# Optimization experiments

Hardware: AMD Instinct MI355X
Metric: run time of the kernel (lower is better)

Reference implementation:

```python
import jax, jax.numpy as jnp
import numpy as np

DIM = 1024
HEADS = 16
HEAD_DIM = DIM // HEADS
HIDDEN = 4 * DIM
EPS = 1e-5


def _layernorm(x, g, b):
    m = jnp.mean(x, axis=-1, keepdims=True)
    v = jnp.mean((x - m) ** 2, axis=-1, keepdims=True)
    return (x - m) * jax.lax.rsqrt(v + EPS) * g + b


def setup_inputs() -> dict:
    key = jax.random.key(0)
    ks = jax.random.split(key, 8)
    s = 0.02
    return {
        "x": jax.random.normal(ks[0], (16, 577, DIM), dtype=jnp.float32),
        "w_qkv": jax.random.normal(ks[1], (3 * DIM, DIM), dtype=jnp.float32) * s,
        "b_qkv": jnp.zeros((3 * DIM,), dtype=jnp.float32),
        "w_proj": jax.random.normal(ks[2], (DIM, DIM), dtype=jnp.float32) * s,
        "b_proj": jnp.zeros((DIM,), dtype=jnp.float32),
        "ln1_g": jnp.ones((DIM,), dtype=jnp.float32),
        "ln1_b": jnp.zeros((DIM,), dtype=jnp.float32),
        "ln2_g": jnp.ones((DIM,), dtype=jnp.float32),
        "ln2_b": jnp.zeros((DIM,), dtype=jnp.float32),
        "w_fc1": jax.random.normal(ks[3], (HIDDEN, DIM), dtype=jnp.float32) * s,
        "b_fc1": jnp.zeros((HIDDEN,), dtype=jnp.float32),
        "w_fc2": jax.random.normal(ks[4], (DIM, HIDDEN), dtype=jnp.float32) * s,
        "b_fc2": jnp.zeros((DIM,), dtype=jnp.float32),
    }


def reference(x, w_qkv, b_qkv, w_proj, b_proj, ln1_g, ln1_b, ln2_g, ln2_b,
              w_fc1, b_fc1, w_fc2, b_fc2):
    B, N, C = x.shape
    scale = HEAD_DIM ** -0.5
    # --- attention sub-block ---
    xn = _layernorm(x, ln1_g, ln1_b)
    qkv = xn @ w_qkv.T + b_qkv  # [B, N, 3C]
    qkv = qkv.reshape(B, N, 3, HEADS, HEAD_DIM)
    q = qkv[:, :, 0].transpose(0, 2, 1, 3)  # [B, H, N, D]
    k = qkv[:, :, 1].transpose(0, 2, 1, 3)
    v = qkv[:, :, 2].transpose(0, 2, 1, 3)
    attn = jnp.einsum('bhnd,bhmd->bhnm', q, k) * scale
    attn = jax.nn.softmax(attn, axis=-1)
    y = jnp.einsum('bhnm,bhmd->bhnd', attn, v)  # [B, H, N, D]
    y = y.transpose(0, 2, 1, 3).reshape(B, N, C)
    y = y @ w_proj.T + b_proj
    x = x + y
    # --- MLP sub-block ---
    xn2 = _layernorm(x, ln2_g, ln2_b)
    h = jax.nn.gelu(xn2 @ w_fc1.T + b_fc1, approximate=False)
    x = x + (h @ w_fc2.T + b_fc2)
    return x
```

## Files before the change

kernel.cpp:

```cpp
#include <hip/hip_runtime.h>
#include <cmath>


#define MTOK 9232
#define MPAD 9344
#define MT_TILES 73
#define SEQ  577
#define SEQP 640
#define NKT  10

typedef _Float16 half8  __attribute__((ext_vector_type(8)));
typedef _Float16 half4  __attribute__((ext_vector_type(4)));
typedef _Float16 half2v __attribute__((ext_vector_type(2)));
typedef __fp16   fp16x2 __attribute__((ext_vector_type(2)));
typedef float    float4v __attribute__((ext_vector_type(4)));

__device__ __forceinline__ void gl_lds16(const void* g, void* l) {
  __builtin_amdgcn_global_load_lds((const __attribute__((address_space(1))) void*)g,
                                   (__attribute__((address_space(3))) void*)l, 16, 0, 0);
}

__device__ __forceinline__ float fexp2(float x) { return __builtin_amdgcn_exp2f(x); }
__device__ __forceinline__ float frcp(float x)  { return __builtin_amdgcn_rcpf(x); }
__device__ __forceinline__ float bperm_f(int addr, float v) {
  return __int_as_float(__builtin_amdgcn_ds_bpermute(addr, __float_as_int(v)));
}
__device__ __forceinline__ half2v pack2(float a, float b) {
  fp16x2 p = __builtin_amdgcn_cvt_pkrtz(a, b);
  return __builtin_bit_cast(half2v, p);
}

__global__ __launch_bounds__(256) void cvt_all_kernel(const float* __restrict__ s0, _Float16* __restrict__ d0,
                                                      const float* __restrict__ s1, _Float16* __restrict__ d1,
                                                      const float* __restrict__ s2, _Float16* __restrict__ d2,
                                                      const float* __restrict__ s3, _Float16* __restrict__ d3) {
  int blk = blockIdx.x;
  const float* in; _Float16* out; int base;
  if (blk < 1536)      { in = s0; out = d0; base = blk; }
  else if (blk < 2048) { in = s1; out = d1; base = blk - 1536; }
  else if (blk < 4096) { in = s2; out = d2; base = blk - 2048; }
  else                 { in = s3; out = d3; base = blk - 4096; }
  int i = (base * 256 + threadIdx.x) * 8;
  float4v a = *(const float4v*)(in + i);
  float4v b = *(const float4v*)(in + i + 4);
  half8 o = { (_Float16)a[0], (_Float16)a[1], (_Float16)a[2], (_Float16)a[3],
              (_Float16)b[0], (_Float16)b[1], (_Float16)b[2], (_Float16)b[3] };
  *(half8*)(out + i) = o;
}

__global__ __launch_bounds__(256) void ln_kernel(const float* __restrict__ x,
                                                 const float* __restrict__ gam,
                                                 const float* __restrict__ bet,
                                                 _Float16* __restrict__ out, int mrows) {
  int row = blockIdx.x, t = threadIdx.x;
  _Float16* orow = out + (long)row * 1024 + t * 4;
  if (row >= mrows) { half4 z = {}; *(half4*)orow = z; return; }
  float4v xv = *(const float4v*)(x + (long)row * 1024 + t * 4);
  float s  = xv[0] + xv[1] + xv[2] + xv[3];
  float ss = xv[0]*xv[0] + xv[1]*xv[1] + xv[2]*xv[2] + xv[3]*xv[3];
  #pragma unroll
  for (int o = 32; o > 0; o >>= 1) { s += __shfl_down(s, o); ss += __shfl_down(ss, o); }
  __shared__ float red[8];
  int w = t >> 6;
  if ((t & 63) == 0) { red[w] = s; red[4 + w] = ss; }
  __syncthreads();
  s  = red[0] + red[1] + red[2] + red[3];
  ss = red[4] + red[5] + red[6] + red[7];
  float mean = s * (1.0f / 1024.0f);
  float var  = ss * (1.0f / 1024.0f) - mean * mean;
  float rstd = rsqrtf(var + 1e-5f);
  float4v gv = *(const float4v*)(gam + t * 4);
  float4v bv = *(const float4v*)(bet + t * 4);
  half4 o;
  #pragma unroll
  for (int i = 0; i < 4; i++) o[i] = (_Float16)((xv[i] - mean) * rstd * gv[i] + bv[i]);
  *(half4*)orow = o;
}

template <int EPI, int DBUF>
__global__ __launch_bounds__(256, DBUF ? 2 : 3)
void gemm_bt(const _Float16* __restrict__ A,
             const _Float16* __restrict__ Bw,
             const float* __restrict__ bias,
             const float* __restrict__ res,
             void* __restrict__ outv, int Ndim, int K) {
  __shared__ __align__(16) _Float16 SH[DBUF ? 32768 : 16384];
  const int GM = 16;
  int nTiles = Ndim >> 7;
  int per = GM * nTiles;
  int lin = blockIdx.x;
  int panel = lin / per;
  int rem = lin - panel * per;
  int gm = MT_TILES - panel * GM; if (gm > GM) gm = GM;
  int mt = panel * GM + rem % gm;
  int nt = rem / gm;
  int t = threadIdx.x, w = t >> 6, l = t & 63;
  int wm = (w >> 1) * 64, wn = (w & 1) * 64;
  int g = l >> 4, li = l & 15;
  float4v acc[4][4] = {};

  long soff[4];
  #pragma unroll
  for (int r = 0; r < 4; ++r) {
    int idx = (w * 4 + r) * 64 + l;
    int row = idx >> 3;
    int kc  = (idx & 7) ^ (row & 7);
    soff[r] = (long)row * K + kc * 8;
  }
  int aro[2][4], bro[2][4];
  #pragma unroll
  for (int ks = 0; ks < 2; ++ks) {
    #pragma unroll
    for (int i = 0; i < 4; ++i) {
      int ar = wm + i * 16 + li;
      aro[ks][i] = ar * 64 + (((ks * 4 + g) ^ (ar & 7)) * 8);
      int br = wn + i * 16 + li;
      bro[ks][i] = br * 64 + (((ks * 4 + g) ^ (br & 7)) * 8);
    }
  }

  const _Float16* ak = A  + (long)mt * 128 * K;
  const _Float16* bk = Bw + (long)nt * 128 * K;
  int nk = K >> 6;

  if (DBUF) {
    #pragma unroll
    for (int r = 0; r < 4; ++r) {
      gl_lds16(ak + soff[r], SH + (w * 4 + r) * 512);
      gl_lds16(bk + soff[r], SH + 8192 + (w * 4 + r) * 512);
    }
    ak += 64; bk += 64;
    for (int kt = 0; kt < nk; ++kt) {
      __syncthreads();
      int coff = (kt & 1) ? 16384 : 0;
      int noff = coff ^ 16384;
      if (kt + 1 < nk) {
        #pragma unroll
        for (int r = 0; r < 4; ++r) {
          gl_lds16(ak + soff[r], SH + noff + (w * 4 + r) * 512);
          gl_lds16(bk + soff[r], SH + noff + 8192 + (w * 4 + r) * 512);
        }
        ak += 64; bk += 64;
      }
      #pragma unroll
      for (int ks = 0; ks < 2; ++ks) {
        half8 af[4], bf[4];
        #pragma unroll
        for (int i = 0; i < 4; i++) af[i] = *(const half8*)(SH + coff + aro[ks][i]);
        #pragma unroll
        for (int j = 0; j < 4; j++) bf[j] = *(const half8*)(SH + coff + 8192 + bro[ks][j]);
        #pragma unroll
        for (int i = 0; i < 4; i++)
          #pragma unroll
          for (int j = 0; j < 4; j++)
            acc[i][j] = __builtin_amdgcn_mfma_f32_16x16x32_f16(af[i], bf[j], acc[i][j], 0, 0, 0);
      }
    }
    __syncthreads();
  } else {
    for (int kt = 0; kt < nk; ++kt) {
      #pragma unroll
      for (int r = 0; r < 4; ++r) {
        gl_lds16(ak + soff[r], SH + (w * 4 + r) * 512);
        gl_lds16(bk + soff[r], SH + 8192 + (w * 4 + r) * 512);
      }
      ak += 64; bk += 64;
      __syncthreads();
      #pragma unroll
      for (int ks = 0; ks < 2; ++ks) {
        half8 af[4], bf[4];
        #pragma unroll
        for (int i = 0; i < 4; i++) af[i] = *(const half8*)(SH + aro[ks][i]);
        #pragma unroll
        for (int j = 0; j < 4; j++) bf[j] = *(const half8*)(SH + 8192 + bro[ks][j]);
        #pragma unroll
        for (int i = 0; i < 4; i++)
          #pragma unroll
          for (int j = 0; j < 4; j++)
            acc[i][j] = __builtin_amdgcn_mfma_f32_16x16x32_f16(af[i], bf[j], acc[i][j], 0, 0, 0);
      }
      __syncthreads();
    }
  }

  if (EPI == 2) {
    float* Shf = (float*)SH;
    #pragma unroll
    for (int p = 0; p < 4; ++p) {
      if ((w & 1) == (p >> 1)) {
        int j0 = (p & 1) * 2;
        #pragma unroll
        for (int i = 0; i < 4; ++i) {
          #pragma unroll
          for (int jj = 0; jj < 2; ++jj) {
            #pragma unroll
            for (int r = 0; r < 4; ++r) {
              int row = wm + i * 16 + g * 4 + r;
              Shf[row * 36 + jj * 16 + li] = acc[i][j0 + jj][r];
            }
          }
        }
      }
      __syncthreads();
      #pragma unroll
      for (int it = 0; it < 4; ++it) {
        int chunk = it * 256 + t;
        int row = chunk >> 3, c4 = chunk & 7;
        int grow = mt * 128 + row;
        if (grow < MTOK) {
          float4v v = *(const float4v*)(Shf + row * 36 + c4 * 4);
          int gcol = nt * 128 + p * 32 + c4 * 4;
          float4v bv = *(const float4v*)(bias + gcol);
          float4v rv = *(const float4v*)(res + (long)grow * Ndim + gcol);
          v = v + bv + rv;
          *(float4v*)((float*)outv + (long)grow * Ndim + gcol) = v;
        }
      }
      __syncthreads();
    }
  } else {
    _Float16* Sh = SH;
    float bsv[4];
    #pragma unroll
    for (int j = 0; j < 4; ++j) bsv[j] = bias[nt * 128 + wn + j * 16 + li];
    #pragma unroll
    for (int p = 0; p < 2; ++p) {
      if ((w & 1) == p) {
        #pragma unroll
        for (int i = 0; i < 4; ++i) {
          int rl = (w >> 1) * 64 + i * 16 + g * 4;
          #pragma unroll
          for (int j = 0; j < 4; ++j) {
            #pragma unroll
            for (int r = 0; r < 4; ++r) {
              float v = acc[i][j][r] + bsv[j];
              if (EPI == 1) {
                float y = v * (0.79788456f + 0.035677408f * v * v);
                v = v * frcp(1.0f + fexp2(-2.88539008f * y));
              }
              Sh[(rl + r) * 68 + j * 16 + li] = (_Float16)v;
            }
          }
        }
      }
      __syncthreads();
      #pragma unroll
      for (int cc = 0; cc < 4; ++cc) {
        int chunk = cc * 256 + t;
        int row = chunk >> 3, kc8 = chunk & 7;
        half8 hv = *(const half8*)(Sh + row * 68 + kc8 * 8);
        *(half8*)((_Float16*)outv + (long)(mt * 128 + row) * Ndim + nt * 128 + p * 64 + kc8 * 8) = hv;
      }
      __syncthreads();
    }
  }
}

__global__ __launch_bounds__(256) void vt_kernel(const _Float16* __restrict__ qkv,
                                                 _Float16* __restrict__ Vt) {
  int kt = blockIdx.x, bh = blockIdx.y;
  int b = bh >> 4, h = bh & 15;
  long base = (long)b * SEQ;
  __shared__ _Float16 Lt[64][72];
  int t = threadIdx.x;
  #pragma unroll
  for (int c = t; c < 512; c += 256) {
    int key = c >> 3, dc = c & 7;
    int kglob = kt * 64 + key;
    half8 v = {};
    if (kglob < SEQ) v = *(const half8*)(qkv + (base + kglob) * 3072 + 2048 + h * 64 + dc * 8);
    *(half8*)(&Lt[key][dc * 8]) = v;
  }
  __syncthreads();
  #pragma unroll
  for (int c = t; c < 512; c += 256) {
    int d = c >> 3, kc = c & 7;
    half8 o;
    #pragma unroll
    for (int j = 0; j < 8; j++) o[j] = Lt[kc * 8 + j][d];
    *(half8*)(Vt + ((long)bh * 64 + d) * SEQP + kt * 64 + kc * 8) = o;
  }
}

__global__ __launch_bounds__(256, 4) void attn_kernel(const _Float16* __restrict__ qkv,
                                                      const _Float16* __restrict__ Vt,
                                                      _Float16* __restrict__ Y) {
  int bh = blockIdx.x, qt = blockIdx.y;
  int b = bh >> 4, h = bh & 15;
  long base = (long)b * SEQ;
  int t = threadIdx.x, w = t >> 6, l = t & 63;
  int g = l >> 4, li = l & 15;
  __shared__ __align__(16) _Float16 Ks[64 * 64];
  __shared__ __align__(16) _Float16 Vs[64 * 64];
  __shared__ __align__(16) _Float16 Pw[4][16 * 40];
  int q0 = qt * 64 + w * 16;
  half8 qf[2];
  #pragma unroll
  for (int ks = 0; ks < 2; ++ks)
    qf[ks] = *(const half8*)(qkv + (base + q0 + li) * 3072 + h * 64 + ks * 32 + g * 8);
  float4v o[4] = {};
  float mold = -1e30f, lsum = 0.f;
  int abase = (l & 48);
  const _Float16* vtb = Vt + (long)bh * 64 * SEQP;
  const float sc = 0.125f * 1.44269504f;
  for (int kt = 0; kt < NKT; ++kt) {
    #pragma unroll
    for (int rr = 0; rr < 2; ++rr) {
      int idx = rr * 256 + w * 64 + l;
      int row = idx >> 3;
      int kc  = (idx & 7) ^ (row & 7);
      gl_lds16(qkv + (base + kt * 64 + row) * 3072 + 1024 + h * 64 + kc * 8,
               Ks + (rr * 256 + w * 64) * 8);
      gl_lds16(vtb + (long)row * SEQP + kt * 64 + kc * 8,
               Vs + (rr * 256 + w * 64) * 8);
    }
    __syncthreads();
    float4v st[4] = {};
    #pragma unroll
    for (int ks = 0; ks < 2; ++ks) {
      #pragma unroll
      for (int mt = 0; mt < 4; ++mt) {
        int kr = mt * 16 + li;
        half8 kf = *(const half8*)(Ks + kr * 64 + (((ks * 4 + g) ^ (kr & 7)) * 8));
        st[mt] = __builtin_amdgcn_mfma_f32_16x16x32_f16(kf, qf[ks], st[mt], 0, 0, 0);
      }
    }
    bool last = (kt == NKT - 1);
    float mx = -1e30f;
    #pragma unroll
    for (int mt = 0; mt < 4; ++mt) {
      #pragma unroll
      for (int r = 0; r < 4; ++r) {
        float v = st[mt][r] * sc;
        if (last && (kt * 64 + mt * 16 + g * 4 + r) >= SEQ) v = -1e30f;
        st[mt][r] = v;
        mx = fmaxf(mx, v);
      }
    }
    mx = fmaxf(mx, __shfl_xor(mx, 16));
    mx = fmaxf(mx, __shfl_xor(mx, 32));
    float mnew = fmaxf(mold, mx);
    float alpha = fexp2(mold - mnew);
    mold = mnew;
    half2v pk[4][2];
    float psum = 0.f;
    #pragma unroll
    for (int mt = 0; mt < 4; ++mt) {
      float p0 = fexp2(st[mt][0] - mnew);
      float p1 = fexp2(st[mt][1] - mnew);
      float p2 = fexp2(st[mt][2] - mnew);
      float p3 = fexp2(st[mt][3] - mnew);
      psum += (p0 + p1) + (p2 + p3);
      pk[mt][0] = pack2(p0, p1);
      pk[mt][1] = pack2(p2, p3);
    }
    lsum = lsum * alpha + psum;
    float ab[4];
    #pragma unroll
    for (int r = 0; r < 4; ++r) ab[r] = bperm_f(abase + 4 * r, alpha);
    #pragma unroll
    for (int nd = 0; nd < 4; ++nd)
      #pragma unroll
      for (int r = 0; r < 4; ++r) o[nd][r] *= ab[r];
    #pragma unroll
    for (int ks = 0; ks < 2; ++ks) {
      #pragma unroll
      for (int mtl = 0; mtl < 2; ++mtl) {
        int mt = 2 * ks + mtl;
        *(half2v*)(&Pw[w][li * 40 + mtl * 16 + g * 4])     = pk[mt][0];
        *(half2v*)(&Pw[w][li * 40 + mtl * 16 + g * 4 + 2]) = pk[mt][1];
      }
      half8 pa = *(const half8*)(&Pw[w][li * 40 + g * 8]);
      #pragma unroll
      for (int nd = 0; nd < 4; ++nd) {
        int vr = nd * 16 + li;
        half8 vf = *(const half8*)(Vs + vr * 64 + (((ks * 4 + g) ^ (vr & 7)) * 8));
        o[nd] = __builtin_amdgcn_mfma_f32_16x16x32_f16(pa, vf, o[nd], 0, 0, 0);
      }
    }
    __syncthreads();
  }
  lsum += __shfl_xor(lsum, 16);
  lsum += __shfl_xor(lsum, 32);
  float linv = frcp(lsum);
  float lb[4];
  #pragma unroll
  for (int r = 0; r < 4; ++r) lb[r] = bperm_f(abase + 4 * r, linv);
  #pragma unroll
  for (int r = 0; r < 4; ++r) {
    int qr = qt * 64 + w * 16 + g * 4 + r;
    if (qr < SEQ) {
      _Float16* yp = Y + (base + qr) * 1024 + h * 64 + li;
      #pragma unroll
      for (int nd = 0; nd < 4; ++nd) yp[nd * 16] = (_Float16)(o[nd][r] * lb[r]);
    }
  }
}

extern "C" void kernel_launch(void* const* d_in, const int* in_sizes, int n_in,
                              void* d_out, int out_size, void* d_ws, size_t ws_size,
                              hipStream_t stream) {
  (void)in_sizes; (void)n_in; (void)out_size; (void)ws_size;
  const float* x      = (const float*)d_in[0];
  const float* w_qkv  = (const float*)d_in[1];
  const float* b_qkv  = (const float*)d_in[2];
  const float* w_proj = (const float*)d_in[3];
  const float* b_proj = (const float*)d_in[4];
  const float* ln1_g  = (const float*)d_in[5];
  const float* ln1_b  = (const float*)d_in[6];
  const float* ln2_g  = (const float*)d_in[7];
  const float* ln2_b  = (const float*)d_in[8];
  const float* w_fc1  = (const float*)d_in[9];
  const float* b_fc1  = (const float*)d_in[10];
  const float* w_fc2  = (const float*)d_in[11];
  const float* b_fc2  = (const float*)d_in[12];

  char* ws = (char*)d_ws;
  _Float16* Abuf = (_Float16*)ws;
  _Float16* Wq   = (_Float16*)(ws + 19136512);
  _Float16* Wp   = Wq + 3072 * 1024;
  _Float16* W1   = Wp + 1024 * 1024;
  _Float16* W2   = W1 + 4096 * 1024;
  _Float16* Qb   = (_Float16*)(ws + 44302336);
  _Float16* Yb   = Qb + (long)MPAD * 3072;
  _Float16* Hb   = Qb;
  float*    X1   = (float*)(ws + 120848384);
  _Float16* Vtb  = (_Float16*)(ws + 120848384);

  cvt_all_kernel<<<6144, 256, 0, stream>>>(w_qkv, Wq, w_proj, Wp, w_fc1, W1, w_fc2, W2);

  ln_kernel<<<MPAD, 256, 0, stream>>>(x, ln1_g, ln1_b, Abuf, MTOK);
  gemm_bt<0, 0><<<73 * 24, 256, 0, stream>>>(Abuf, Wq, b_qkv, nullptr, Qb, 3072, 1024);
  vt_kernel<<<dim3(NKT, 256), 256, 0, stream>>>(Qb, Vtb);
  attn_kernel<<<dim3(256, NKT), 256, 0, stream>>>(Qb, Vtb, Yb);
  gemm_bt<2, 1><<<73 * 8, 256, 0, stream>>>(Yb, Wp, b_proj, x, X1, 1024, 1024);
  ln_kernel<<<MPAD, 256, 0, stream>>>(X1, ln2_g, ln2_b, Abuf, MTOK);
  gemm_bt<1, 0><<<73 * 32, 256, 0, stream>>>(Abuf, W1, b_fc1, nullptr, Hb, 4096, 1024);
  gemm_bt<2, 1><<<73 * 8, 256, 0, stream>>>(Hb, W2, b_fc2, X1, d_out, 1024, 4096);
}
```

Measured before the change: 552.2 us.

## Use 128x64 single-buffered tiles for N=1024 residual GEMMs

Adds a new GEMM kernel with 128x64 output tiles, smaller LDS, and four blocks per CU for the proj and fc2 GEMMs. It replaces the double-buffered 128x128 variant and doubles the block count (73*16 instead of 73*8) so the 256 CUs are better filled. The aim is to fix low occupancy and wave quantization on the N=1024 GEMMs. The cost is losing the double-buffered prefetch and re-reading A tiles more often.

```diff
diff --git a/kernel.cpp b/kernel.cpp
--- a/kernel.cpp
+++ b/kernel.cpp
@@ -77,14 +77,12 @@
   *(half4*)orow = o;
 }
 
-template <int EPI, int DBUF>
-__global__ __launch_bounds__(256, DBUF ? 2 : 3)
-void gemm_bt(const _Float16* __restrict__ A,
-             const _Float16* __restrict__ Bw,
-             const float* __restrict__ bias,
-             const float* __restrict__ res,
-             void* __restrict__ outv, int Ndim, int K) {
-  __shared__ __align__(16) _Float16 SH[DBUF ? 32768 : 16384];
+template <int EPI>
+__global__ __launch_bounds__(256, 3) void gemm_bt(const _Float16* __restrict__ A,
+                                                  const _Float16* __restrict__ Bw,
+                                                  const float* __restrict__ bias,
+                                                  void* __restrict__ outv, int Ndim, int K) {
+  __shared__ __align__(16) _Float16 SH[16384];
   const int GM = 16;
   int nTiles = Ndim >> 7;
   int per = GM * nTiles;
@@ -122,137 +120,172 @@
   const _Float16* ak = A  + (long)mt * 128 * K;
   const _Float16* bk = Bw + (long)nt * 128 * K;
   int nk = K >> 6;
-
-  if (DBUF) {
+  for (int kt = 0; kt < nk; ++kt) {
     #pragma unroll
     for (int r = 0; r < 4; ++r) {
       gl_lds16(ak + soff[r], SH + (w * 4 + r) * 512);
       gl_lds16(bk + soff[r], SH + 8192 + (w * 4 + r) * 512);
     }
     ak += 64; bk += 64;
-    for (int kt = 0; kt < nk; ++kt) {
-      __syncthreads();
-      int coff = (kt & 1) ? 16384 : 0;
-      int noff = coff ^ 16384;
-      if (kt + 1 < nk) {
+    __syncthreads();
+    #pragma unroll
+    for (int ks = 0; ks < 2; ++ks) {
+      half8 af[4], bf[4];
+      #pragma unroll
+      for (int i = 0; i < 4; i++) af[i] = *(const half8*)(SH + aro[ks][i]);
+      #pragma unroll
+      for (int j = 0; j < 4; j++) bf[j] = *(const half8*)(SH + 8192 + bro[ks][j]);
+      #pragma unroll
+      for (int i = 0; i < 4; i++)
         #pragma unroll
-        for (int r = 0; r < 4; ++r) {
-          gl_lds16(ak + soff[r], SH + noff + (w * 4 + r) * 512);
-          gl_lds16(bk + soff[r], SH + noff + 8192 + (w * 4 + r) * 512);
-        }
-        ak += 64; bk += 64;
-      }
-      #pragma unroll
-      for (int ks = 0; ks < 2; ++ks) {
-        half8 af[4], bf[4];
+        for (int j = 0; j < 4; j++)
+          acc[i][j] = __builtin_amdgcn_mfma_f32_16x16x32_f16(af[i], bf[j], acc[i][j], 0, 0, 0);
+    }
+    __syncthreads();
+  }
+  _Float16* Sh = SH;
+  float bsv[4];
+  #pragma unroll
+  for (int j = 0; j < 4; ++j) bsv[j] = bias[nt * 128 + wn + j * 16 + li];
+  #pragma unroll
+  for (int p = 0; p < 2; ++p) {
+    if ((w & 1) == p) {
+      #pragma unroll
+      for (int i = 0; i < 4; ++i) {
+        int rl = (w >> 1) * 64 + i * 16 + g * 4;
         #pragma unroll
-        for (int i = 0; i < 4; i++) af[i] = *(const half8*)(SH + coff + aro[ks][i]);
-        #pragma unroll
-        for (int j = 0; j < 4; j++) bf[j] = *(const half8*)(SH + coff + 8192 + bro[ks][j]);
-        #pragma unroll
-        for (int i = 0; i < 4; i++)
+        for (int j = 0; j < 4; ++j) {
           #pragma unroll
-          for (int j = 0; j < 4; j++)
-            acc[i][j] = __builtin_amdgcn_mfma_f32_16x16x32_f16(af[i], bf[j], acc[i][j], 0, 0, 0);
-      }
-    }
-    __syncthreads();
-  } else {
-    for (int kt = 0; kt < nk; ++kt) {
-      #pragma unroll
-      for (int r = 0; r < 4; ++r) {
-        gl_lds16(ak + soff[r], SH + (w * 4 + r) * 512);
-        gl_lds16(bk + soff[r], SH + 8192 + (w * 4 + r) * 512);
-      }
-      ak += 64; bk += 64;
-      __syncthreads();
-      #pragma unroll
-      for (int ks = 0; ks < 2; ++ks) {
-        half8 af[4], bf[4];
-        #pragma unroll
-        for (int i = 0; i < 4; i++) af[i] = *(const half8*)(SH + aro[ks][i]);
-        #pragma unroll
-        for (int j = 0; j < 4; j++) bf[j] = *(const half8*)(SH + 8192 + bro[ks][j]);
-        #pragma unroll
-        for (int i = 0; i < 4; i++)
-          #pragma unroll
-          for (int j = 0; j < 4; j++)
-            acc[i][j] = __builtin_amdgcn_mfma_f32_16x16x32_f16(af[i], bf[j], acc[i][j], 0, 0, 0);
-      }
-      __syncthreads();
-    }
-  }
-
-  if (EPI == 2) {
-    float* Shf = (float*)SH;
-    #pragma unroll
-    for (int p = 0; p < 4; ++p) {
-      if ((w & 1) == (p >> 1)) {
-        int j0 = (p & 1) * 2;
-        #pragma unroll
-        for (int i = 0; i < 4; ++i) {
-          #pragma unroll
-          for (int jj = 0; jj < 2; ++jj) {
-            #pragma unroll
-            for (int r = 0; r < 4; ++r) {
-              int row = wm + i * 16 + g * 4 + r;
-              Shf[row * 36 + jj * 16 + li] = acc[i][j0 + jj][r];
+          for (int r = 0; r < 4; ++r) {
+            float v = acc[i][j][r] + bsv[j];
+            if (EPI == 1) {
+              float y = v * (0.79788456f + 0.035677408f * v * v);
+              v = v * frcp(1.0f + fexp2(-2.88539008f * y));
             }
+            Sh[(rl + r) * 68 + j * 16 + li] = (_Float16)v;
           }
         }
       }
-      __syncthreads();
-      #pragma unroll
-      for (int it = 0; it < 4; ++it) {
-        int chunk = it * 256 + t;
-        int row = chunk >> 3, c4 = chunk & 7;
-        int grow = mt * 128 + row;
-        if (grow < MTOK) {
-          float4v v = *(const float4v*)(Shf + row * 36 + c4 * 4);
-          int gcol = nt * 128 + p * 32 + c4 * 4;
-          float4v bv = *(const float4v*)(bias + gcol);
-          float4v rv = *(const float4v*)(res + (long)grow * Ndim + gcol);
-          v = v + bv + rv;
-          *(float4v*)((float*)outv + (long)grow * Ndim + gcol) = v;
-        }
-      }
-      __syncthreads();
-    }
-  } else {
-    _Float16* Sh = SH;
-    float bsv[4];
-    #pragma unroll
-    for (int j = 0; j < 4; ++j) bsv[j] = bias[nt * 128 + wn + j * 16 + li];
-    #pragma unroll
-    for (int p = 0; p < 2; ++p) {
-      if ((w & 1) == p) {
+    }
+    __syncthreads();
+    #pragma unroll
+    for (int cc = 0; cc < 4; ++cc) {
+      int chunk = cc * 256 + t;
+      int row = chunk >> 3, kc8 = chunk & 7;
+      half8 hv = *(const half8*)(Sh + row * 68 + kc8 * 8);
+      *(half8*)((_Float16*)outv + (long)(mt * 128 + row) * Ndim + nt * 128 + p * 64 + kc8 * 8) = hv;
+    }
+    __syncthreads();
+  }
+}
+
+__global__ __launch_bounds__(256, 4) void gemm_bt64(const _Float16* __restrict__ A,
+                                                    const _Float16* __restrict__ Bw,
+                                                    const float* __restrict__ bias,
+                                                    const float* __restrict__ res,
+                                                    float* __restrict__ outv, int Ndim, int K) {
+  __shared__ __align__(16) _Float16 SH[12288];
+  const int GM = 16;
+  int nTiles = Ndim >> 6;
+  int per = GM * nTiles;
+  int lin = blockIdx.x;
+  int panel = lin / per;
+  int rem = lin - panel * per;
+  int gm = MT_TILES - panel * GM; if (gm > GM) gm = GM;
+  int mt = panel * GM + rem % gm;
+  int nt = rem / gm;
+  int t = threadIdx.x, w = t >> 6, l = t & 63;
+  int wm = (w >> 1) * 64, wn = (w & 1) * 32;
+  int g = l >> 4, li = l & 15;
+  float4v acc[4][2] = {};
+
+  long soffA[4], soffB[2];
+  #pragma unroll
+  for (int r = 0; r < 4; ++r) {
+    int idx = (w * 4 + r) * 64 + l;
+    int row = idx >> 3;
+    int kc  = (idx & 7) ^ (row & 7);
+    soffA[r] = (long)row * K + kc * 8;
+  }
+  #pragma unroll
+  for (int r = 0; r < 2; ++r) {
+    int idx = (w * 2 + r) * 64 + l;
+    int row = idx >> 3;
+    int kc  = (idx & 7) ^ (row & 7);
+    soffB[r] = (long)row * K + kc * 8;
+  }
+  int aro[2][4], bro[2][2];
+  #pragma unroll
+  for (int ks = 0; ks < 2; ++ks) {
+    #pragma unroll
+    for (int i = 0; i < 4; ++i) {
+      int ar = wm + i * 16 + li;
+      aro[ks][i] = ar * 64 + (((ks * 4 + g) ^ (ar & 7)) * 8);
+    }
+    #pragma unroll
+    for (int j = 0; j < 2; ++j) {
+      int br = wn + j * 16 + li;
+      bro[ks][j] = br * 64 + (((ks * 4 + g) ^ (br & 7)) * 8);
+    }
+  }
+
+  const _Float16* ak = A  + (long)mt * 128 * K;
+  const _Float16* bk = Bw + (long)nt * 64 * K;
+  int nk = K >> 6;
+  for (int kt = 0; kt < nk; ++kt) {
+    #pragma unroll
+    for (int r = 0; r < 4; ++r) gl_lds16(ak + soffA[r], SH + (w * 4 + r) * 512);
+    #pragma unroll
+    for (int r = 0; r < 2; ++r) gl_lds16(bk + soffB[r], SH + 8192 + (w * 2 + r) * 512);
+    ak += 64; bk += 64;
+    __syncthreads();
+    #pragma unroll
+    for (int ks = 0; ks < 2; ++ks) {
+      half8 af[4], bf[2];
+      #pragma unroll
+      for (int i = 0; i < 4; i++) af[i] = *(const half8*)(SH + aro[ks][i]);
+      #pragma unroll
+      for (int j = 0; j < 2; j++) bf[j] = *(const half8*)(SH + 8192 + bro[ks][j]);
+      #pragma unroll
+      for (int i = 0; i < 4; i++)
         #pragma unroll
-        for (int i = 0; i < 4; ++i) {
-          int rl = (w >> 1) * 64 + i * 16 + g * 4;
+        for (int j = 0; j < 2; j++)
+          acc[i][j] = __builtin_amdgcn_mfma_f32_16x16x32_f16(af[i], bf[j], acc[i][j], 0, 0, 0);
+    }
+    __syncthreads();
+  }
+  float* Shf = (float*)SH;
+  #pragma unroll
+  for (int p = 0; p < 2; ++p) {
+    if ((w & 1) == p) {
+      #pragma unroll
+      for (int i = 0; i < 4; ++i) {
+        #pragma unroll
+        for (int j = 0; j < 2; ++j) {
           #pragma unroll
-          for (int j = 0; j < 4; ++j) {
-            #pragma unroll
-            for (int r = 0; r < 4; ++r) {
-              float v = acc[i][j][r] + bsv[j];
-              if (EPI == 1) {
-                float y = v * (0.79788456f + 0.035677408f * v * v);
-                v = v * frcp(1.0f + fexp2(-2.88539008f * y));
-              }
-              Sh[(rl + r) * 68 + j * 16 + li] = (_Float16)v;
-            }
+          for (int r = 0; r < 4; ++r) {
+            int row = wm + i * 16 + g * 4 + r;
+            Shf[row * 36 + j * 16 + li] = acc[i][j][r];
           }
         }
       }
-      __syncthreads();
-      #pragma unroll
-      for (int cc = 0; cc < 4; ++cc) {
-        int chunk = cc * 256 + t;
-        int row = chunk >> 3, kc8 = chunk & 7;
-        half8 hv = *(const half8*)(Sh + row * 68 + kc8 * 8);
-        *(half8*)((_Float16*)outv + (long)(mt * 128 + row) * Ndim + nt * 128 + p * 64 + kc8 * 8) = hv;
-      }
-      __syncthreads();
-    }
+    }
+    __syncthreads();
+    #pragma unroll
+    for (int it = 0; it < 4; ++it) {
+      int chunk = it * 256 + t;
+      int row = chunk >> 3, c4 = chunk & 7;
+      int grow = mt * 128 + row;
+      if (grow < MTOK) {
+        float4v v = *(const float4v*)(Shf + row * 36 + c4 * 4);
+        int gcol = nt * 64 + p * 32 + c4 * 4;
+        float4v bv = *(const float4v*)(bias + gcol);
+        float4v rv = *(const float4v*)(res + (long)grow * Ndim + gcol);
+        v = v + bv + rv;
+        *(float4v*)(outv + (long)grow * Ndim + gcol) = v;
+      }
+    }
+    __syncthreads();
   }
 }
 
@@ -430,11 +463,11 @@
   cvt_all_kernel<<<6144, 256, 0, stream>>>(w_qkv, Wq, w_proj, Wp, w_fc1, W1, w_fc2, W2);
 
   ln_kernel<<<MPAD, 256, 0, stream>>>(x, ln1_g, ln1_b, Abuf, MTOK);
-  gemm_bt<0, 0><<<73 * 24, 256, 0, stream>>>(Abuf, Wq, b_qkv, nullptr, Qb, 3072, 1024);
+  gemm_bt<0><<<73 * 24, 256, 0, stream>>>(Abuf, Wq, b_qkv, Qb, 3072, 1024);
   vt_kernel<<<dim3(NKT, 256), 256, 0, stream>>>(Qb, Vtb);
   attn_kernel<<<dim3(256, NKT), 256, 0, stream>>>(Qb, Vtb, Yb);
-  gemm_bt<2, 1><<<73 * 8, 256, 0, stream>>>(Yb, Wp, b_proj, x, X1, 1024, 1024);
+  gemm_bt64<<<73 * 16, 256, 0, stream>>>(Yb, Wp, b_proj, x, X1, 1024, 1024);
   ln_kernel<<<MPAD, 256, 0, stream>>>(X1, ln2_g, ln2_b, Abuf, MTOK);
-  gemm_bt<1, 0><<<73 * 32, 256, 0, stream>>>(Abuf, W1, b_fc1, nullptr, Hb, 4096, 1024);
-  gemm_bt<2, 1><<<73 * 8, 256, 0, stream>>>(Hb, W2, b_fc2, X1, d_out, 1024, 4096);
-}
+  gemm_bt<1><<<73 * 32, 256, 0, stream>>>(Abuf, W1, b_fc1, Hb, 4096, 1024);
+  gemm_bt64<<<73 * 16, 256, 0, stream>>>(Hb, W2, b_fc2, X1, (float*)d_out, 1024, 4096);
+}
```

After: 516.5 us. -6.5%, faster.
